# Kernel optimization log

Measured on AMD Instinct MI355X. Metric: run time of the kernel, lower is better.

## Reference

```python
import jax, jax.numpy as jnp
import numpy as np

B, H, S, HD = 4, 8, 2048, 64   # batch, heads, seq, head_dim (num_out_feats//num_heads)
D_IN = 512                      # num_in_feats (projector output width)
D_CAT = H * HD                  # projector input width


def setup_inputs() -> dict:
    key = jax.random.key(0)
    kq, kk, kv, kw, kb = jax.random.split(key, 5)
    q = jax.random.normal(kq, (B, H, S, HD), dtype=jnp.float32)
    k = jax.random.normal(kk, (B, H, S, HD), dtype=jnp.float32)
    v = jax.random.normal(kv, (B, H, S, HD), dtype=jnp.float32)
    # torch Linear(D_CAT, D_IN): weight [D_IN, D_CAT], bias [D_IN]
    W = jax.random.normal(kw, (D_IN, D_CAT), dtype=jnp.float32) * 0.02
    bias = jax.random.normal(kb, (D_IN,), dtype=jnp.float32) * 0.02
    return {"q": q, "k": k, "v": v, "W": W, "bias": bias}


def reference(q, k, v, W, bias):
    head_dim = q.shape[-1]
    scale = jnp.asarray(1.0 / np.sqrt(head_dim), dtype=q.dtype)
    # scores: [b, h, sq, sk], single stable softmax
    scores = jax.nn.softmax(jnp.einsum('bhqd,bhkd->bhqk', q, k) * scale, axis=-1)
    # AV: the original broadcast-multiply-sum is mathematically a matmul
    o = jnp.einsum('bhqk,bhkd->bhqd', scores, v)  # [b, h, s, hd]
    b, h, s, d = o.shape
    # faithful to torch .view(b, s, -1) on a contiguous [b,h,s,d] buffer: raw reshape (no head transpose)
    o = o.reshape(b, s, h * d)
    return o @ W.T + bias
```

## Files before the change

kernel.cpp:

```cpp
#include <hip/hip_runtime.h>

#define BATCH 4
#define NH    8
#define SEQ   2048
#define HDIM  64
#define DIN   512
#define DCAT  512
#define NBH   (BATCH*NH)
#define NT    32

typedef __attribute__((ext_vector_type(8))) short short8;
typedef __attribute__((ext_vector_type(4))) float f32x4;
typedef __attribute__((ext_vector_type(4))) unsigned int uint4v;
typedef __attribute__((ext_vector_type(2))) unsigned int uint2v;
typedef unsigned short u16;
typedef unsigned int u32;

__device__ inline u32 cvtpk(float lo, float hi) {
    u32 r;
    asm("v_cvt_pk_bf16_f32 %0, %1, %2" : "=v"(r) : "v"(lo), "v"(hi));
    return r;
}

__device__ inline void glds16(const void* g, void* l) {
    __builtin_amdgcn_global_load_lds(
        (const __attribute__((address_space(1))) u32*)g,
        (__attribute__((address_space(3))) u32*)l, 16, 0, 0);
}

__global__ __launch_bounds__(256)
void vt_prepass(const float* __restrict__ vg, u16* __restrict__ vt) {
    const int bh = blockIdx.x, tb = blockIdx.y, t = threadIdx.x;
    __shared__ float Ls[32][65];
    const float* vp = vg + ((size_t)bh * SEQ + tb * 32) * HDIM;
    {
        int r = t >> 3, c8 = (t & 7) * 8;
        float4 f0 = *reinterpret_cast<const float4*>(vp + r * HDIM + c8);
        float4 f1 = *reinterpret_cast<const float4*>(vp + r * HDIM + c8 + 4);
        Ls[r][c8+0] = f0.x; Ls[r][c8+1] = f0.y; Ls[r][c8+2] = f0.z; Ls[r][c8+3] = f0.w;
        Ls[r][c8+4] = f1.x; Ls[r][c8+5] = f1.y; Ls[r][c8+6] = f1.z; Ls[r][c8+7] = f1.w;
    }
    __syncthreads();
    u16* wt = vt + ((size_t)bh * 64 + tb) * 2048;
    {
        int d = t >> 2, p = t & 3;
        int j0 = (p ^ (d & 3)) * 8;
        uint4v u;
        u.x = cvtpk(Ls[j0+0][d], Ls[j0+1][d]);
        u.y = cvtpk(Ls[j0+2][d], Ls[j0+3][d]);
        u.z = cvtpk(Ls[j0+4][d], Ls[j0+5][d]);
        u.w = cvtpk(Ls[j0+6][d], Ls[j0+7][d]);
        *reinterpret_cast<uint4v*>(wt + d * 32 + p * 8) = u;
    }
}

__global__ __launch_bounds__(512, 4)
void attn_mfma(const float* __restrict__ qg, const float* __restrict__ kg,
               const u16* __restrict__ vtg, u16* __restrict__ og) {
    const int bh  = blockIdx.x;
    const int qB  = blockIdx.y * 128;
    const int tid = threadIdx.x;
    const int w = tid >> 6, lane = tid & 63;
    const int qc = w & 3, half = w >> 2;
    const int c = lane & 15, g = lane >> 4;

    __shared__ char sh[53248];
    auto Kb = [&](int h, int b) { return sh + (h*2 + b) * 4096; };
    auto Vb = [&](int h, int b) { return sh + 16384 + (h*2 + b) * 4096; };
    u16* const Pw = (u16*)(sh + 32768 + w * 2560);

    const size_t base = (size_t)bh * SEQ * HDIM;

    const float qs = 0.125f * 1.44269504088896f;
    short8 qb[2][2];
#pragma unroll
    for (int qt = 0; qt < 2; ++qt)
#pragma unroll
    for (int ds = 0; ds < 2; ++ds) {
        const float* qp = qg + base + (size_t)(qB + qc*32 + qt*16 + c) * HDIM + ds*32 + g*8;
        float4 f0 = *reinterpret_cast<const float4*>(qp);
        float4 f1 = *reinterpret_cast<const float4*>(qp + 4);
        uint4v u;
        u.x = cvtpk(f0.x * qs, f0.y * qs);
        u.y = cvtpk(f0.z * qs, f0.w * qs);
        u.z = cvtpk(f1.x * qs, f1.y * qs);
        u.w = cvtpk(f1.z * qs, f1.w * qs);
        qb[qt][ds] = __builtin_bit_cast(short8, u);
    }

    const int srow = tid >> 4;
    const int sp4  = tid & 15;
    const int kwoff = srow*128 + ((((sp4 >> 1) ^ (srow & 7)) << 4) | ((sp4 & 1) << 3));
    const float* kgp0 = kg + base + (size_t)srow * HDIM + sp4 * 4;
    const float* kgp1 = kgp0 + (size_t)1024 * HDIM;
    const int vh  = tid >> 8;
    const int vls = (tid & 255) * 16;
    const u16* vsrc = vtg + (size_t)bh * 64 * 2048 + (size_t)(vh * 32) * 2048 + (tid & 255) * 8;

    f32x4 ot[2][4];
#pragma unroll
    for (int qt = 0; qt < 2; ++qt)
#pragma unroll
    for (int dt = 0; dt < 4; ++dt) ot[qt][dt] = (f32x4){0.f,0.f,0.f,0.f};
    float l[2] = {0.f, 0.f};

    float4 kr0, kr1;
    kr0 = *reinterpret_cast<const float4*>(kgp0);
    kr1 = *reinterpret_cast<const float4*>(kgp1);
    glds16(vsrc, Vb(vh, 0) + vls);
    {
        uint2v u0, u1;
        u0.x = cvtpk(kr0.x, kr0.y); u0.y = cvtpk(kr0.z, kr0.w);
        u1.x = cvtpk(kr1.x, kr1.y); u1.y = cvtpk(kr1.z, kr1.w);
        *reinterpret_cast<uint2v*>(Kb(0,0) + kwoff) = u0;
        *reinterpret_cast<uint2v*>(Kb(1,0) + kwoff) = u1;
    }
    kr0 = *reinterpret_cast<const float4*>(kgp0 + 2048);
    kr1 = *reinterpret_cast<const float4*>(kgp1 + 2048);
    asm volatile("s_waitcnt vmcnt(2) lgkmcnt(0)" ::: "memory");
    __builtin_amdgcn_s_barrier();
    glds16(vsrc + 2048, Vb(vh, 1) + vls);

    for (int t = 0; t < NT; ++t) {
        const int b = t & 1;
        const char* Kc = Kb(half, b);
        const char* Vc = Vb(half, b);

        f32x4 st[2][2];
#pragma unroll
        for (int qt = 0; qt < 2; ++qt)
#pragma unroll
        for (int kvt = 0; kvt < 2; ++kvt) st[qt][kvt] = (f32x4){0.f,0.f,0.f,0.f};
        __builtin_amdgcn_s_setprio(1);
#pragma unroll
        for (int kvt = 0; kvt < 2; ++kvt)
#pragma unroll
        for (int ds = 0; ds < 2; ++ds) {
            short8 ka = *reinterpret_cast<const short8*>(
                Kc + (kvt*16 + c)*128 + (((ds*4 + g) ^ (c & 7)) << 4));
            st[0][kvt] = __builtin_amdgcn_mfma_f32_16x16x32_bf16(ka, qb[0][ds], st[0][kvt], 0,0,0);
            st[1][kvt] = __builtin_amdgcn_mfma_f32_16x16x32_bf16(ka, qb[1][ds], st[1][kvt], 0,0,0);
        }
        __builtin_amdgcn_s_setprio(0);

#pragma unroll
        for (int qt = 0; qt < 2; ++qt) {
            float lp = 0.f;
#pragma unroll
            for (int kvt = 0; kvt < 2; ++kvt) {
                float p0 = __builtin_amdgcn_exp2f(st[qt][kvt][0]);
                float p1 = __builtin_amdgcn_exp2f(st[qt][kvt][1]);
                float p2 = __builtin_amdgcn_exp2f(st[qt][kvt][2]);
                float p3 = __builtin_amdgcn_exp2f(st[qt][kvt][3]);
                lp += (p0 + p1) + (p2 + p3);
                uint2v pw;
                pw.x = cvtpk(p0, p1);
                pw.y = cvtpk(p2, p3);
                *reinterpret_cast<uint2v*>(Pw + (qt*16 + c)*40 + kvt*16 + g*4) = pw;
            }
            l[qt] += lp;
        }

        short8 pb0 = *reinterpret_cast<const short8*>(Pw + c*40 + g*8);
        short8 pb1 = *reinterpret_cast<const short8*>(Pw + (16 + c)*40 + g*8);
        __builtin_amdgcn_s_setprio(1);
#pragma unroll
        for (int dt = 0; dt < 4; ++dt) {
            short8 va = *reinterpret_cast<const short8*>(
                Vc + (dt*16 + c)*64 + ((g ^ (c & 3)) << 4));
            ot[0][dt] = __builtin_amdgcn_mfma_f32_16x16x32_bf16(va, pb0, ot[0][dt], 0,0,0);
            ot[1][dt] = __builtin_amdgcn_mfma_f32_16x16x32_bf16(va, pb1, ot[1][dt], 0,0,0);
        }
        __builtin_amdgcn_s_setprio(0);

        if (t + 1 < NT) {
            uint2v u0, u1;
            u0.x = cvtpk(kr0.x, kr0.y); u0.y = cvtpk(kr0.z, kr0.w);
            u1.x = cvtpk(kr1.x, kr1.y); u1.y = cvtpk(kr1.z, kr1.w);
            *reinterpret_cast<uint2v*>(Kb(0, b ^ 1) + kwoff) = u0;
            *reinterpret_cast<uint2v*>(Kb(1, b ^ 1) + kwoff) = u1;
        }
        if (t + 2 < NT) {
            kr0 = *reinterpret_cast<const float4*>(kgp0 + (size_t)(t + 2) * 2048);
            kr1 = *reinterpret_cast<const float4*>(kgp1 + (size_t)(t + 2) * 2048);
        }
        if (t < NT - 2)
            asm volatile("s_waitcnt vmcnt(2) lgkmcnt(0)" ::: "memory");
        else
            asm volatile("s_waitcnt vmcnt(0) lgkmcnt(0)" ::: "memory");
        __builtin_amdgcn_s_barrier();
        if (t + 2 < NT)
            glds16(vsrc + (size_t)(t + 2) * 2048, Vb(vh, b) + vls);
    }

#pragma unroll
    for (int qt = 0; qt < 2; ++qt) {
        l[qt] += __shfl_xor(l[qt], 16);
        l[qt] += __shfl_xor(l[qt], 32);
    }
    if (w >= 4) {
        char* area = sh + (w & 3) * 8192;
#pragma unroll
        for (int qt = 0; qt < 2; ++qt)
#pragma unroll
        for (int dt = 0; dt < 4; ++dt)
            *reinterpret_cast<f32x4*>(area + lane*128 + ((((qt*4+dt) ^ (lane & 7)) << 4))) = ot[qt][dt];
        float* fl = (float*)(sh + 32768 + w * 2560);
        fl[lane*2]   = l[0];
        fl[lane*2+1] = l[1];
    }
    __syncthreads();
    if (w < 4) {
        char* area = sh + w * 8192;
        const float* fl = (const float*)(sh + 32768 + (w + 4) * 2560);
        float l0 = l[0] + fl[lane*2];
        float l1 = l[1] + fl[lane*2+1];
        float inv[2] = {1.0f / l0, 1.0f / l1};
        f32x4 of[2][4];
#pragma unroll
        for (int qt = 0; qt < 2; ++qt)
#pragma unroll
        for (int dt = 0; dt < 4; ++dt) {
            f32x4 po = *reinterpret_cast<const f32x4*>(
                area + lane*128 + ((((qt*4+dt) ^ (lane & 7)) << 4)));
            of[qt][dt] = ot[qt][dt] + po;
        }
        asm volatile("s_waitcnt lgkmcnt(0)" ::: "memory");
#pragma unroll
        for (int qt = 0; qt < 2; ++qt)
#pragma unroll
        for (int dt = 0; dt < 4; ++dt) {
            int r = qt*16 + c, hs = dt*4 + g;
            uint2v o;
            o.x = cvtpk(of[qt][dt][0] * inv[qt], of[qt][dt][1] * inv[qt]);
            o.y = cvtpk(of[qt][dt][2] * inv[qt], of[qt][dt][3] * inv[qt]);
            *reinterpret_cast<uint2v*>(
                area + r*128 + ((((hs >> 1) ^ (r & 7)) << 4) | ((hs & 1) << 3))) = o;
        }
#pragma unroll
        for (int s = 0; s < 4; ++s) {
            int idx = lane + s*64;
            int r = idx >> 3, j = idx & 7;
            uint4v u = *reinterpret_cast<const uint4v*>(area + r*128 + ((j ^ (r & 7)) << 4));
            *reinterpret_cast<uint4v*>(
                og + ((size_t)bh * SEQ + qB + w*32 + r) * HDIM + j*8) = u;
        }
    }
}

__global__ __launch_bounds__(256)
void proj_mfma(const u16* __restrict__ X, const float* __restrict__ Wg,
               const float* __restrict__ bias, float* __restrict__ out) {
    const int g0 = blockIdx.x * 128;
    const int n0 = blockIdx.y * 64;
    const int tid = threadIdx.x;
    const int w = tid >> 6, lane = tid & 63;
    const int c = lane & 15, gq = lane >> 4;
    const int cx = c & 7;

    __shared__ char sh[49152];
    u16* const XbA = (u16*)(sh);
    u16* const XbB = (u16*)(sh + 16384);
    u16* const WbA = (u16*)(sh + 32768);
    u16* const WbB = (u16*)(sh + 40960);

    const int wn0 = tid >> 3, wp = tid & 7;

    f32x4 acc[2][4];
#pragma unroll
    for (int mt = 0; mt < 2; ++mt)
#pragma unroll
    for (int nt = 0; nt < 4; ++nt) acc[mt][nt] = (f32x4){0.f,0.f,0.f,0.f};

    float4 w0a, w0b, w1a, w1b;

    auto loadW = [&](int kt) {
        const float* p0 = Wg + (size_t)(n0 + wn0) * DCAT + kt*64 + ((wp ^ (wn0 & 7)) * 8);
        const float* p1 = Wg + (size_t)(n0 + 32 + wn0) * DCAT + kt*64 + ((wp ^ ((32 + wn0) & 7)) * 8);
        w0a = *reinterpret_cast<const float4*>(p0);
        w0b = *reinterpret_cast<const float4*>(p0 + 4);
        w1a = *reinterpret_cast<const float4*>(p1);
        w1b = *reinterpret_cast<const float4*>(p1 + 4);
    };
    auto writeW = [&](u16* Wb) {
        uint4v u;
        u.x = cvtpk(w0a.x, w0a.y); u.y = cvtpk(w0a.z, w0a.w);
        u.z = cvtpk(w0b.x, w0b.y); u.w = cvtpk(w0b.z, w0b.w);
        *reinterpret_cast<uint4v*>((char*)Wb + wn0*128 + wp*16) = u;
        u.x = cvtpk(w1a.x, w1a.y); u.y = cvtpk(w1a.z, w1a.w);
        u.z = cvtpk(w1b.x, w1b.y); u.w = cvtpk(w1b.z, w1b.w);
        *reinterpret_cast<uint4v*>((char*)Wb + (32 + wn0)*128 + wp*16) = u;
    };
    auto issueX = [&](int kt, u16* Xb) {
#pragma unroll
        for (int i = 0; i < 4; ++i) {
            int s = w*256 + i*64 + lane;
            int r = s >> 3, p = s & 7;
            glds16(X + (size_t)(g0 + r) * DCAT + kt*64 + ((p ^ (r & 7)) * 8),
                   (char*)Xb + w*4096 + i*1024);
        }
    };

    loadW(0);
    issueX(0, XbA);
    writeW(WbA);
    loadW(1);
    issueX(1, XbB);
    asm volatile("s_waitcnt vmcnt(8) lgkmcnt(0)" ::: "memory");
    __builtin_amdgcn_s_barrier();

    for (int kt = 0; kt < 8; ++kt) {
        u16* const Xc = (kt & 1) ? XbB : XbA;
        u16* const Wc = (kt & 1) ? WbB : WbA;
        u16* const Wn = (kt & 1) ? WbA : WbB;

        __builtin_amdgcn_s_setprio(1);
#pragma unroll
        for (int ks = 0; ks < 2; ++ks) {
            short8 a0 = *reinterpret_cast<const short8*>(
                (char*)Xc + (w*32 + c)*128 + (((ks*4 + gq) ^ cx) << 4));
            short8 a1 = *reinterpret_cast<const short8*>(
                (char*)Xc + (w*32 + 16 + c)*128 + (((ks*4 + gq) ^ cx) << 4));
#pragma unroll
            for (int nt = 0; nt < 4; ++nt) {
                short8 bb = *reinterpret_cast<const short8*>(
                    (char*)Wc + (nt*16 + c)*128 + (((ks*4 + gq) ^ cx) << 4));
                acc[0][nt] = __builtin_amdgcn_mfma_f32_16x16x32_bf16(a0, bb, acc[0][nt], 0,0,0);
                acc[1][nt] = __builtin_amdgcn_mfma_f32_16x16x32_bf16(a1, bb, acc[1][nt], 0,0,0);
            }
        }
        __builtin_amdgcn_s_setprio(0);

        if (kt + 1 < 8) writeW(Wn);
        if (kt + 2 < 8) loadW(kt + 2);
        if (kt < 6)
            asm volatile("s_waitcnt vmcnt(4) lgkmcnt(0)" ::: "memory");
        else
            asm volatile("s_waitcnt vmcnt(0) lgkmcnt(0)" ::: "memory");
        __builtin_amdgcn_s_barrier();
        if (kt + 2 < 8) issueX(kt + 2, Xc);
    }

    float bv[4];
#pragma unroll
    for (int nt = 0; nt < 4; ++nt) bv[nt] = bias[n0 + nt*16 + c];
#pragma unroll
    for (int mt = 0; mt < 2; ++mt)
#pragma unroll
    for (int nt = 0; nt < 4; ++nt)
#pragma unroll
    for (int r = 0; r < 4; ++r)
        out[(size_t)(g0 + w*32 + mt*16 + gq*4 + r) * DIN + n0 + nt*16 + c] =
            acc[mt][nt][r] + bv[nt];
}

extern "C" void kernel_launch(void* const* d_in, const int* in_sizes, int n_in,
                              void* d_out, int out_size, void* d_ws, size_t ws_size,
                              hipStream_t stream) {
    (void)in_sizes; (void)n_in; (void)out_size; (void)ws_size;
    const float* q    = (const float*)d_in[0];
    const float* k    = (const float*)d_in[1];
    const float* v    = (const float*)d_in[2];
    const float* W    = (const float*)d_in[3];
    const float* bias = (const float*)d_in[4];

    u16* vt = (u16*)d_ws;
    u16* ob = vt + (size_t)NBH * 64 * 2048;

    vt_prepass<<<dim3(NBH, 64), 256, 0, stream>>>(v, vt);
    attn_mfma <<<dim3(NBH, SEQ/128), 512, 0, stream>>>(q, k, vt, ob);
    proj_mfma <<<dim3((BATCH*SEQ)/128, DIN/64), 256, 0, stream>>>(ob, W, bias, (float*)d_out);
}
```

Before: 68.62 us.

## Switch attention to 32x32x16 MFMA and pass P through lane shuffles, not LDS

Replaces the 16x16x32 bf16 MFMA tiling in the attention kernel with 32x32x16 MFMAs, so each wave computes a 32x32 score tile with one accumulator. The softmax probabilities are moved into the B-operand layout with cross-half lane shuffles instead of a per-wave LDS round trip, which cuts LDS use and the shared-memory footprint. The V prepass layout and its swizzle change to match the new operand access, and the epilogue is rewritten for the new accumulator layout. The aim is fewer MFMA issues and less LDS traffic per tile, at the cost of extra shuffles and selects and a more complex register layout.

```diff
diff --git a/kernel.cpp b/kernel.cpp
--- a/kernel.cpp
+++ b/kernel.cpp
@@ -11,10 +11,13 @@
 
 typedef __attribute__((ext_vector_type(8))) short short8;
 typedef __attribute__((ext_vector_type(4))) float f32x4;
+typedef __attribute__((ext_vector_type(16))) float f32x16;
 typedef __attribute__((ext_vector_type(4))) unsigned int uint4v;
 typedef __attribute__((ext_vector_type(2))) unsigned int uint2v;
 typedef unsigned short u16;
 typedef unsigned int u32;
+
+#define ZERO16 (f32x16){0.f,0.f,0.f,0.f,0.f,0.f,0.f,0.f,0.f,0.f,0.f,0.f,0.f,0.f,0.f,0.f}
 
 __device__ inline u32 cvtpk(float lo, float hi) {
     u32 r;
@@ -43,14 +46,16 @@
     __syncthreads();
     u16* wt = vt + ((size_t)bh * 64 + tb) * 2048;
     {
-        int d = t >> 2, p = t & 3;
-        int j0 = (p ^ (d & 3)) * 8;
+        int r = t >> 3, p = t & 7;
+        int sL = p ^ (r & 7);
+        int d  = (sL >> 2) * 32 + r;
+        int j0 = (sL & 3) * 8;
         uint4v u;
         u.x = cvtpk(Ls[j0+0][d], Ls[j0+1][d]);
         u.y = cvtpk(Ls[j0+2][d], Ls[j0+3][d]);
         u.z = cvtpk(Ls[j0+4][d], Ls[j0+5][d]);
         u.w = cvtpk(Ls[j0+6][d], Ls[j0+7][d]);
-        *reinterpret_cast<uint4v*>(wt + d * 32 + p * 8) = u;
+        *reinterpret_cast<uint4v*>(wt + r * 64 + p * 8) = u;
     }
 }
 
@@ -62,22 +67,21 @@
     const int tid = threadIdx.x;
     const int w = tid >> 6, lane = tid & 63;
     const int qc = w & 3, half = w >> 2;
-    const int c = lane & 15, g = lane >> 4;
-
-    __shared__ char sh[53248];
+    const int r  = lane & 31;
+    const int hi = lane >> 5;
+    const bool hib = hi != 0;
+
+    __shared__ char sh[33792];
     auto Kb = [&](int h, int b) { return sh + (h*2 + b) * 4096; };
     auto Vb = [&](int h, int b) { return sh + 16384 + (h*2 + b) * 4096; };
-    u16* const Pw = (u16*)(sh + 32768 + w * 2560);
 
     const size_t base = (size_t)bh * SEQ * HDIM;
 
     const float qs = 0.125f * 1.44269504088896f;
-    short8 qb[2][2];
-#pragma unroll
-    for (int qt = 0; qt < 2; ++qt)
-#pragma unroll
-    for (int ds = 0; ds < 2; ++ds) {
-        const float* qp = qg + base + (size_t)(qB + qc*32 + qt*16 + c) * HDIM + ds*32 + g*8;
+    short8 qb[4];
+#pragma unroll
+    for (int ks = 0; ks < 4; ++ks) {
+        const float* qp = qg + base + (size_t)(qB + qc*32 + r) * HDIM + ks*16 + hi*8;
         float4 f0 = *reinterpret_cast<const float4*>(qp);
         float4 f1 = *reinterpret_cast<const float4*>(qp + 4);
         uint4v u;
@@ -85,7 +89,7 @@
         u.y = cvtpk(f0.z * qs, f0.w * qs);
         u.z = cvtpk(f1.x * qs, f1.y * qs);
         u.w = cvtpk(f1.z * qs, f1.w * qs);
-        qb[qt][ds] = __builtin_bit_cast(short8, u);
+        qb[ks] = __builtin_bit_cast(short8, u);
     }
 
     const int srow = tid >> 4;
@@ -97,12 +101,8 @@
     const int vls = (tid & 255) * 16;
     const u16* vsrc = vtg + (size_t)bh * 64 * 2048 + (size_t)(vh * 32) * 2048 + (tid & 255) * 8;
 
-    f32x4 ot[2][4];
-#pragma unroll
-    for (int qt = 0; qt < 2; ++qt)
-#pragma unroll
-    for (int dt = 0; dt < 4; ++dt) ot[qt][dt] = (f32x4){0.f,0.f,0.f,0.f};
-    float l[2] = {0.f, 0.f};
+    f32x16 ot[2] = { ZERO16, ZERO16 };
+    float l = 0.f;
 
     float4 kr0, kr1;
     kr0 = *reinterpret_cast<const float4*>(kgp0);
@@ -126,50 +126,46 @@
         const char* Kc = Kb(half, b);
         const char* Vc = Vb(half, b);
 
-        f32x4 st[2][2];
-#pragma unroll
-        for (int qt = 0; qt < 2; ++qt)
-#pragma unroll
-        for (int kvt = 0; kvt < 2; ++kvt) st[qt][kvt] = (f32x4){0.f,0.f,0.f,0.f};
+        f32x16 st = ZERO16;
         __builtin_amdgcn_s_setprio(1);
 #pragma unroll
-        for (int kvt = 0; kvt < 2; ++kvt)
-#pragma unroll
-        for (int ds = 0; ds < 2; ++ds) {
+        for (int ks = 0; ks < 4; ++ks) {
             short8 ka = *reinterpret_cast<const short8*>(
-                Kc + (kvt*16 + c)*128 + (((ds*4 + g) ^ (c & 7)) << 4));
-            st[0][kvt] = __builtin_amdgcn_mfma_f32_16x16x32_bf16(ka, qb[0][ds], st[0][kvt], 0,0,0);
-            st[1][kvt] = __builtin_amdgcn_mfma_f32_16x16x32_bf16(ka, qb[1][ds], st[1][kvt], 0,0,0);
+                Kc + r*128 + (((ks*2 + hi) ^ (r & 7)) << 4));
+            st = __builtin_amdgcn_mfma_f32_32x32x16_bf16(ka, qb[ks], st, 0, 0, 0);
         }
         __builtin_amdgcn_s_setprio(0);
 
-#pragma unroll
-        for (int qt = 0; qt < 2; ++qt) {
-            float lp = 0.f;
-#pragma unroll
-            for (int kvt = 0; kvt < 2; ++kvt) {
-                float p0 = __builtin_amdgcn_exp2f(st[qt][kvt][0]);
-                float p1 = __builtin_amdgcn_exp2f(st[qt][kvt][1]);
-                float p2 = __builtin_amdgcn_exp2f(st[qt][kvt][2]);
-                float p3 = __builtin_amdgcn_exp2f(st[qt][kvt][3]);
-                lp += (p0 + p1) + (p2 + p3);
-                uint2v pw;
-                pw.x = cvtpk(p0, p1);
-                pw.y = cvtpk(p2, p3);
-                *reinterpret_cast<uint2v*>(Pw + (qt*16 + c)*40 + kvt*16 + g*4) = pw;
-            }
-            l[qt] += lp;
-        }
-
-        short8 pb0 = *reinterpret_cast<const short8*>(Pw + c*40 + g*8);
-        short8 pb1 = *reinterpret_cast<const short8*>(Pw + (16 + c)*40 + g*8);
+        u32 pw[8];
+        float lp = 0.f;
+#pragma unroll
+        for (int j = 0; j < 8; ++j) {
+            float p0 = __builtin_amdgcn_exp2f(st[2*j]);
+            float p1 = __builtin_amdgcn_exp2f(st[2*j+1]);
+            lp += p0 + p1;
+            pw[j] = cvtpk(p0, p1);
+        }
+        l += lp;
+
+        u32 xw[8];
+#pragma unroll
+        for (int j = 0; j < 8; ++j) xw[j] = (u32)__shfl_xor((int)pw[j], 32);
+
+        uint4v b0, b1;
+        b0.x = hib ? xw[2] : pw[0];  b0.y = hib ? xw[3] : pw[1];
+        b0.z = hib ? pw[2] : xw[0];  b0.w = hib ? pw[3] : xw[1];
+        b1.x = hib ? xw[6] : pw[4];  b1.y = hib ? xw[7] : pw[5];
+        b1.z = hib ? pw[6] : xw[4];  b1.w = hib ? pw[7] : xw[5];
+        short8 pb[2] = { __builtin_bit_cast(short8, b0), __builtin_bit_cast(short8, b1) };
+
         __builtin_amdgcn_s_setprio(1);
 #pragma unroll
-        for (int dt = 0; dt < 4; ++dt) {
+        for (int dt = 0; dt < 2; ++dt)
+#pragma unroll
+        for (int ks = 0; ks < 2; ++ks) {
             short8 va = *reinterpret_cast<const short8*>(
-                Vc + (dt*16 + c)*64 + ((g ^ (c & 3)) << 4));
-            ot[0][dt] = __builtin_amdgcn_mfma_f32_16x16x32_bf16(va, pb0, ot[0][dt], 0,0,0);
-            ot[1][dt] = __builtin_amdgcn_mfma_f32_16x16x32_bf16(va, pb1, ot[1][dt], 0,0,0);
+                Vc + r*128 + (((dt*4 + ks*2 + hi) ^ (r & 7)) << 4));
+            ot[dt] = __builtin_amdgcn_mfma_f32_32x32x16_bf16(va, pb[ks], ot[dt], 0, 0, 0);
         }
         __builtin_amdgcn_s_setprio(0);
 
@@ -193,57 +189,52 @@
             glds16(vsrc + (size_t)(t + 2) * 2048, Vb(vh, b) + vls);
     }
 
-#pragma unroll
-    for (int qt = 0; qt < 2; ++qt) {
-        l[qt] += __shfl_xor(l[qt], 16);
-        l[qt] += __shfl_xor(l[qt], 32);
-    }
+    l += __shfl_xor(l, 32);
+
+    float* dumpF = (float*)(sh + (w & 3) * 8192) + lane * 32;
+    float* dumpL = (float*)(sh + 32768) + (w & 3) * 64;
     if (w >= 4) {
-        char* area = sh + (w & 3) * 8192;
-#pragma unroll
-        for (int qt = 0; qt < 2; ++qt)
-#pragma unroll
-        for (int dt = 0; dt < 4; ++dt)
-            *reinterpret_cast<f32x4*>(area + lane*128 + ((((qt*4+dt) ^ (lane & 7)) << 4))) = ot[qt][dt];
-        float* fl = (float*)(sh + 32768 + w * 2560);
-        fl[lane*2]   = l[0];
-        fl[lane*2+1] = l[1];
+#pragma unroll
+        for (int dt = 0; dt < 2; ++dt)
+#pragma unroll
+        for (int jj = 0; jj < 4; ++jj) {
+            f32x4 c = { ot[dt][jj*4+0], ot[dt][jj*4+1], ot[dt][jj*4+2], ot[dt][jj*4+3] };
+            *reinterpret_cast<f32x4*>(dumpF + dt*16 + jj*4) = c;
+        }
+        dumpL[lane] = l;
     }
     __syncthreads();
     if (w < 4) {
-        char* area = sh + w * 8192;
-        const float* fl = (const float*)(sh + 32768 + (w + 4) * 2560);
-        float l0 = l[0] + fl[lane*2];
-        float l1 = l[1] + fl[lane*2+1];
-        float inv[2] = {1.0f / l0, 1.0f / l1};
-        f32x4 of[2][4];
-#pragma unroll
-        for (int qt = 0; qt < 2; ++qt)
-#pragma unroll
-        for (int dt = 0; dt < 4; ++dt) {
-            f32x4 po = *reinterpret_cast<const f32x4*>(
-                area + lane*128 + ((((qt*4+dt) ^ (lane & 7)) << 4)));
-            of[qt][dt] = ot[qt][dt] + po;
-        }
+#pragma unroll
+        for (int dt = 0; dt < 2; ++dt)
+#pragma unroll
+        for (int jj = 0; jj < 4; ++jj) {
+            f32x4 c = *reinterpret_cast<const f32x4*>(dumpF + dt*16 + jj*4);
+            ot[dt][jj*4+0] += c[0]; ot[dt][jj*4+1] += c[1];
+            ot[dt][jj*4+2] += c[2]; ot[dt][jj*4+3] += c[3];
+        }
+        float ltot = l + dumpL[lane];
+        float inv  = 1.0f / ltot;
         asm volatile("s_waitcnt lgkmcnt(0)" ::: "memory");
-#pragma unroll
-        for (int qt = 0; qt < 2; ++qt)
-#pragma unroll
-        for (int dt = 0; dt < 4; ++dt) {
-            int r = qt*16 + c, hs = dt*4 + g;
-            uint2v o;
-            o.x = cvtpk(of[qt][dt][0] * inv[qt], of[qt][dt][1] * inv[qt]);
-            o.y = cvtpk(of[qt][dt][2] * inv[qt], of[qt][dt][3] * inv[qt]);
-            *reinterpret_cast<uint2v*>(
-                area + r*128 + ((((hs >> 1) ^ (r & 7)) << 4) | ((hs & 1) << 3))) = o;
-        }
+        __builtin_amdgcn_sched_barrier(0);
+        u16* ta = (u16*)(sh + w * 8192);
+#pragma unroll
+        for (int dt = 0; dt < 2; ++dt)
+#pragma unroll
+        for (int j = 0; j < 8; ++j) {
+            u32 wd = cvtpk(ot[dt][2*j] * inv, ot[dt][2*j+1] * inv);
+            int d = dt*32 + ((2*j) & 3) + 8*((2*j) >> 2) + 4*hi;
+            *reinterpret_cast<u32*>((char*)ta + r*144 + d*2) = wd;
+        }
+        asm volatile("s_waitcnt lgkmcnt(0)" ::: "memory");
+        __builtin_amdgcn_sched_barrier(0);
 #pragma unroll
         for (int s = 0; s < 4; ++s) {
             int idx = lane + s*64;
-            int r = idx >> 3, j = idx & 7;
-            uint4v u = *reinterpret_cast<const uint4v*>(area + r*128 + ((j ^ (r & 7)) << 4));
+            int rr = idx >> 3, j = idx & 7;
+            uint4v u = *reinterpret_cast<const uint4v*>((char*)ta + rr*144 + j*16);
             *reinterpret_cast<uint4v*>(
-                og + ((size_t)bh * SEQ + qB + w*32 + r) * HDIM + j*8) = u;
+                og + ((size_t)bh * SEQ + qB + w*32 + rr) * HDIM + j*8) = u;
         }
     }
 }
@@ -295,8 +286,8 @@
 #pragma unroll
         for (int i = 0; i < 4; ++i) {
             int s = w*256 + i*64 + lane;
-            int r = s >> 3, p = s & 7;
-            glds16(X + (size_t)(g0 + r) * DCAT + kt*64 + ((p ^ (r & 7)) * 8),
+            int rr = s >> 3, p = s & 7;
+            glds16(X + (size_t)(g0 + rr) * DCAT + kt*64 + ((p ^ (rr & 7)) * 8),
                    (char*)Xb + w*4096 + i*1024);
         }
     };
@@ -349,9 +340,9 @@
 #pragma unroll
     for (int nt = 0; nt < 4; ++nt)
 #pragma unroll
-    for (int r = 0; r < 4; ++r)
-        out[(size_t)(g0 + w*32 + mt*16 + gq*4 + r) * DIN + n0 + nt*16 + c] =
-            acc[mt][nt][r] + bv[nt];
+    for (int rr = 0; rr < 4; ++rr)
+        out[(size_t)(g0 + w*32 + mt*16 + gq*4 + rr) * DIN + n0 + nt*16 + c] =
+            acc[mt][nt][rr] + bv[nt];
 }
 
 extern "C" void kernel_launch(void* const* d_in, const int* in_sizes, int n_in,
```

Measured after the change: 77.13 us. 1.12x slower.
